# Kernel optimization log

Measured on AMD Instinct MI355X. Metric: run time of the kernel, lower is better.

The kernel has to match this reference:

```python
import jax, jax.numpy as jnp
import numpy as np

N_NODES = 50000
N_EDGES = 600000
F_IN = 128
HID = 128
N_CLASSES = 10
N_GRAPHS = 64


def _glorot(key, shape):
    fan_in, fan_out = shape[1], shape[0]
    lim = float(np.sqrt(6.0 / (fan_in + fan_out)))
    return jax.random.uniform(key, shape, jnp.float32, -lim, lim)


def setup_inputs() -> dict:
    key = jax.random.key(0)
    ks = jax.random.split(key, 16)
    x = jax.random.normal(ks[0], (N_NODES, F_IN), jnp.float32)
    edge_index = jax.random.randint(ks[1], (2, N_EDGES), 0, N_NODES, jnp.int64)
    batch = jnp.sort(jax.random.randint(ks[2], (N_NODES,), 0, N_GRAPHS, jnp.int64))
    # GraphConv params: lin_rel (with bias) applied to aggregated neighbor sum,
    # lin_root (no bias) applied to the node's own features.
    params = dict(
        W1_rel=_glorot(ks[3], (HID, F_IN)), b1_rel=jnp.zeros((HID,), jnp.float32),
        W1_root=_glorot(ks[4], (HID, F_IN)),
        W2_rel=_glorot(ks[5], (HID, HID)), b2_rel=jnp.zeros((HID,), jnp.float32),
        W2_root=_glorot(ks[6], (HID, HID)),
        W3_rel=_glorot(ks[7], (HID, HID)), b3_rel=jnp.zeros((HID,), jnp.float32),
        W3_root=_glorot(ks[8], (HID, HID)),
        W_lin=_glorot(ks[9], (N_CLASSES, HID)), b_lin=jnp.zeros((N_CLASSES,), jnp.float32),
    )
    return {"x": x, "edge_index": edge_index, "batch": batch, **params}


def _graph_conv(x, src, dst, W_rel, b_rel, W_root):
    # gather source features, scatter-add into targets, then linear (sum aggr
    # commutes with the linear, matching PyG GraphConv which applies lin_rel
    # after aggregation)
    agg = jax.ops.segment_sum(x[src], dst, num_segments=N_NODES)  # [N, F]
    return agg @ W_rel.T + b_rel + x @ W_root.T


def _mean_pool(x, batch):
    sums = jax.ops.segment_sum(x, batch, num_segments=N_GRAPHS)  # [G, H]
    cnts = jax.ops.segment_sum(jnp.ones((x.shape[0],), x.dtype), batch,
                               num_segments=N_GRAPHS)
    return sums / jnp.maximum(cnts, 1.0)[:, None]


def reference(x, edge_index, batch,
              W1_rel, b1_rel, W1_root,
              W2_rel, b2_rel, W2_root,
              W3_rel, b3_rel, W3_root,
              W_lin, b_lin):
    src, dst = edge_index[0], edge_index[1]
    h = jax.nn.relu(_graph_conv(x, src, dst, W1_rel, b1_rel, W1_root))
    h = jax.nn.relu(_graph_conv(h, src, dst, W2_rel, b2_rel, W2_root))
    h = _graph_conv(h, src, dst, W3_rel, b3_rel, W3_root)
    g = _mean_pool(h, batch)  # [G, H]
    # dropout is identity in eval mode (training=False)
    return g @ W_lin.T + b_lin  # [G, num_classes]
```

## Files before the change

kernel.cpp:

```cpp
#include <hip/hip_runtime.h>
#include <hip/hip_bf16.h>

#define N_NODES   50000
#define N_EDGES   600000
#define F         128
#define N_GRAPHS  64
#define N_CLASSES 10
#define NPAD      50048
#define NB_SCAN   196
#define XCVT_BLOCKS 6250
#define WCVT_BLOCKS 96
#define EDGE_BLOCKS 2344

typedef __attribute__((ext_vector_type(8))) short bf16x8;
typedef __attribute__((ext_vector_type(4))) float f32x4;

static __device__ __forceinline__ unsigned short f2bf(float f) {
    __hip_bfloat16 h = __float2bfloat16(f);
    return *reinterpret_cast<unsigned short*>(&h);
}
static __device__ __forceinline__ float bf2f(unsigned short u) {
    return __uint_as_float(((unsigned)u) << 16);
}

__global__ __launch_bounds__(256) void prep_kernel(
    const float* __restrict__ x,
    const float* __restrict__ W0, const float* __restrict__ W1,
    const float* __restrict__ W2, const float* __restrict__ W3,
    const float* __restrict__ W4, const float* __restrict__ W5,
    const int* __restrict__ dst,
    unsigned short* __restrict__ Xb, unsigned short* __restrict__ Wb,
    int* __restrict__ deg)
{
    int b = blockIdx.x;
    if (b < XCVT_BLOCKS) {
        int i = b * 256 + threadIdx.x;
        float4 v = reinterpret_cast<const float4*>(x)[i];
        ushort4 o;
        o.x = f2bf(v.x); o.y = f2bf(v.y); o.z = f2bf(v.z); o.w = f2bf(v.w);
        reinterpret_cast<ushort4*>(Xb)[i] = o;
    } else if (b < XCVT_BLOCKS + WCVT_BLOCKS) {
        const int PER = (F * F / 4) / 256;
        int bb  = b - XCVT_BLOCKS;
        int mat = bb / PER;
        int i   = (bb % PER) * 256 + threadIdx.x;
        const float* W = (mat == 0) ? W0 : (mat == 1) ? W1 : (mat == 2) ? W2
                       : (mat == 3) ? W3 : (mat == 4) ? W4 : W5;
        float4 v = reinterpret_cast<const float4*>(W)[i];
        ushort4 o;
        o.x = f2bf(v.x); o.y = f2bf(v.y); o.z = f2bf(v.z); o.w = f2bf(v.w);
        reinterpret_cast<ushort4*>(Wb + (size_t)mat * F * F)[i] = o;
    } else {
        int e = (b - XCVT_BLOCKS - WCVT_BLOCKS) * 256 + threadIdx.x;
        if (e < N_EDGES) atomicAdd(&deg[dst[e]], 1);
    }
}

__global__ __launch_bounds__(256) void scanA_kernel(
    const int* __restrict__ deg, int* __restrict__ locEx, int* __restrict__ blockSum)
{
    __shared__ int sh[256];
    int t = threadIdx.x;
    int idx = blockIdx.x * 256 + t;
    int v = (idx < N_NODES) ? deg[idx] : 0;
    sh[t] = v;
    __syncthreads();
#pragma unroll
    for (int d = 1; d < 256; d <<= 1) {
        int u = (t >= d) ? sh[t - d] : 0;
        __syncthreads();
        sh[t] += u;
        __syncthreads();
    }
    if (idx < N_NODES) locEx[idx] = sh[t] - v;
    if (t == 255) blockSum[blockIdx.x] = sh[255];
}

__global__ __launch_bounds__(256) void scanBC_kernel(
    const int* __restrict__ locEx, const int* __restrict__ blockSum,
    int* __restrict__ off)
{
    __shared__ int sh[256];
    int t = threadIdx.x;
    int v = (t < NB_SCAN) ? blockSum[t] : 0;
    sh[t] = v;
    __syncthreads();
#pragma unroll
    for (int d = 1; d < 256; d <<= 1) {
        int u = (t >= d) ? sh[t - d] : 0;
        __syncthreads();
        sh[t] += u;
        __syncthreads();
    }
    int myVal = blockSum[blockIdx.x];
    int base  = sh[blockIdx.x] - myVal;
    int idx = blockIdx.x * 256 + t;
    if (idx < N_NODES) off[idx] = locEx[idx] + base;
    if (blockIdx.x == 0 && t == 0) off[N_NODES] = sh[NB_SCAN - 1];
}

__global__ __launch_bounds__(256) void fillP_kernel(
    const int* __restrict__ src, const int* __restrict__ dst,
    const int* __restrict__ off, int* __restrict__ cursor,
    int* __restrict__ csrP)
{
    int e = blockIdx.x * 256 + threadIdx.x;
    if (e >= N_EDGES) return;
    int d = dst[e];
    int slot = atomicAdd(&cursor[d], 1);
    csrP[off[d] + slot] = src[e];
}

template <int RELU>
__global__ __launch_bounds__(256) void conv_fused(
    const unsigned short* __restrict__ Xb,
    const int* __restrict__ off, const int* __restrict__ csrP,
    const unsigned short* __restrict__ Wrel, const unsigned short* __restrict__ Wroot,
    const float* __restrict__ brel, unsigned short* __restrict__ H)
{
    __shared__ char AsRaw[64 * 256];
    const int t = threadIdx.x;
    const int mBase = blockIdx.x * 64;

    {
        const int r = t >> 2;
        const int q = t & 3;
        int row = mBase + r;
        float acc[32];
#pragma unroll
        for (int i = 0; i < 32; ++i) acc[i] = 0.f;
        if (row < N_NODES) {
            int j0 = off[row], j1 = off[row + 1];
            const int* lst = csrP;
            const unsigned short* Xq = Xb + (size_t)q * 32;
            int j = j0;
            for (; j + 2 <= j1; j += 2) {
                int sa = lst[j], sb = lst[j + 1];
                const bf16x8* pa = reinterpret_cast<const bf16x8*>(Xq + (size_t)sa * F);
                const bf16x8* pb = reinterpret_cast<const bf16x8*>(Xq + (size_t)sb * F);
                bf16x8 va0 = pa[0], va1 = pa[1], va2 = pa[2], va3 = pa[3];
                bf16x8 vb0 = pb[0], vb1 = pb[1], vb2 = pb[2], vb3 = pb[3];
#pragma unroll
                for (int e = 0; e < 8; ++e) {
                    acc[e]      += bf2f((unsigned short)va0[e]) + bf2f((unsigned short)vb0[e]);
                    acc[8 + e]  += bf2f((unsigned short)va1[e]) + bf2f((unsigned short)vb1[e]);
                    acc[16 + e] += bf2f((unsigned short)va2[e]) + bf2f((unsigned short)vb2[e]);
                    acc[24 + e] += bf2f((unsigned short)va3[e]) + bf2f((unsigned short)vb3[e]);
                }
            }
            if (j < j1) {
                int sa = lst[j];
                const bf16x8* pa = reinterpret_cast<const bf16x8*>(Xq + (size_t)sa * F);
                bf16x8 va0 = pa[0], va1 = pa[1], va2 = pa[2], va3 = pa[3];
#pragma unroll
                for (int e = 0; e < 8; ++e) {
                    acc[e]      += bf2f((unsigned short)va0[e]);
                    acc[8 + e]  += bf2f((unsigned short)va1[e]);
                    acc[16 + e] += bf2f((unsigned short)va2[e]);
                    acc[24 + e] += bf2f((unsigned short)va3[e]);
                }
            }
        }
#pragma unroll
        for (int cc = 0; cc < 4; ++cc) {
            bf16x8 o;
#pragma unroll
            for (int e = 0; e < 8; ++e) o[e] = (short)f2bf(acc[cc * 8 + e]);
            int bytecol = (q * 64 + cc * 16) ^ ((r & 7) << 4);
            *reinterpret_cast<bf16x8*>(AsRaw + r * 256 + bytecol) = o;
        }
    }
    __syncthreads();

    const int wave = t >> 6;
    const int lane = t & 63;
    const int wm = wave >> 1, wn = wave & 1;
    const int m0l = wm * 32;
    const int n0  = wn * 64;
    const int lrow = lane & 15;
    const int lk8  = (lane >> 4) << 3;

    f32x4 acc[2][4];
#pragma unroll
    for (int mi = 0; mi < 2; ++mi)
#pragma unroll
        for (int ni = 0; ni < 4; ++ni)
            acc[mi][ni] = (f32x4){0.f, 0.f, 0.f, 0.f};

#pragma unroll
    for (int p = 0; p < 2; ++p) {
        const unsigned short* W = p ? Wroot : Wrel;
#pragma unroll
        for (int ks = 0; ks < 4; ++ks) {
            int k0 = ks * 32 + lk8;
            bf16x8 a[2], b[4];
#pragma unroll
            for (int mi = 0; mi < 2; ++mi) {
                int rl = m0l + mi * 16 + lrow;
                if (p == 0) {
                    int bytecol = (k0 * 2) ^ ((rl & 7) << 4);
                    a[mi] = *reinterpret_cast<const bf16x8*>(AsRaw + rl * 256 + bytecol);
                } else {
                    a[mi] = *reinterpret_cast<const bf16x8*>(
                        Xb + (size_t)(mBase + rl) * F + k0);
                }
            }
#pragma unroll
            for (int ni = 0; ni < 4; ++ni)
                b[ni] = *reinterpret_cast<const bf16x8*>(
                    W + (size_t)(n0 + ni * 16 + lrow) * F + k0);
#pragma unroll
            for (int mi = 0; mi < 2; ++mi)
#pragma unroll
                for (int ni = 0; ni < 4; ++ni)
                    acc[mi][ni] = __builtin_amdgcn_mfma_f32_16x16x32_bf16(
                        a[mi], b[ni], acc[mi][ni], 0, 0, 0);
        }
    }

    const int r0 = (lane >> 4) << 2;
#pragma unroll
    for (int ni = 0; ni < 4; ++ni) {
        int col = n0 + ni * 16 + lrow;
        float bb = brel[col];
#pragma unroll
        for (int mi = 0; mi < 2; ++mi) {
#pragma unroll
            for (int r = 0; r < 4; ++r) {
                int row = mBase + m0l + mi * 16 + r0 + r;
                if (row < N_NODES) {
                    float v = acc[mi][ni][r] + bb;
                    if (RELU) v = fmaxf(v, 0.f);
                    H[(size_t)row * F + col] = f2bf(v);
                }
            }
        }
    }
}

__global__ __launch_bounds__(256) void poolhead_kernel(
    const unsigned short* __restrict__ H, const int* __restrict__ batch,
    const float* __restrict__ Wl, const float* __restrict__ bl,
    float* __restrict__ out)
{
    int g = blockIdx.x;
    int lo = 0, hi = N_NODES;
    while (lo < hi) { int m = (lo + hi) >> 1; if (batch[m] < g) lo = m + 1; else hi = m; }
    int start = lo;
    hi = N_NODES;
    while (lo < hi) { int m = (lo + hi) >> 1; if (batch[m] < g + 1) lo = m + 1; else hi = m; }
    int end = lo;

    int l8 = (threadIdx.x & 15) << 3;
    int rg = threadIdx.x >> 4;
    float acc[8] = {0.f, 0.f, 0.f, 0.f, 0.f, 0.f, 0.f, 0.f};
    for (int i = start + rg; i < end; i += 16) {
        bf16x8 v = *reinterpret_cast<const bf16x8*>(H + (size_t)i * F + l8);
#pragma unroll
        for (int r = 0; r < 8; ++r) acc[r] += bf2f((unsigned short)v[r]);
    }
    __shared__ float sh[16][F];
    __shared__ float mean[F];
#pragma unroll
    for (int r = 0; r < 8; ++r) sh[rg][l8 + r] = acc[r];
    __syncthreads();
    if (threadIdx.x < F) {
        int f = threadIdx.x;
        float s = 0.f;
#pragma unroll
        for (int k = 0; k < 16; ++k) s += sh[k][f];
        float cnt = (float)(end - start);
        mean[f] = s / fmaxf(cnt, 1.f);
    }
    __syncthreads();
    if (threadIdx.x < N_CLASSES) {
        int c = threadIdx.x;
        float s = bl[c];
#pragma unroll 8
        for (int k = 0; k < F; ++k) s += mean[k] * Wl[c * F + k];
        out[g * N_CLASSES + c] = s;
    }
}

extern "C" void kernel_launch(void* const* d_in, const int* in_sizes, int n_in,
                              void* d_out, int out_size, void* d_ws, size_t ws_size,
                              hipStream_t stream)
{
    const float* x     = (const float*)d_in[0];
    const int*   edge  = (const int*)d_in[1];
    const int*   src   = edge;
    const int*   dst   = edge + N_EDGES;
    const int*   batch = (const int*)d_in[2];
    const float* W1r = (const float*)d_in[3];
    const float* b1  = (const float*)d_in[4];
    const float* W1o = (const float*)d_in[5];
    const float* W2r = (const float*)d_in[6];
    const float* b2  = (const float*)d_in[7];
    const float* W2o = (const float*)d_in[8];
    const float* W3r = (const float*)d_in[9];
    const float* b3  = (const float*)d_in[10];
    const float* W3o = (const float*)d_in[11];
    const float* Wl  = (const float*)d_in[12];
    const float* bl  = (const float*)d_in[13];
    float* out = (float*)d_out;

    char* ws = (char*)d_ws;
    const size_t fb = (size_t)NPAD * F * sizeof(unsigned short);
    unsigned short* Xb  = (unsigned short*)ws;
    unsigned short* H1b = (unsigned short*)(ws + fb);
    unsigned short* H2b = (unsigned short*)(ws + 2 * fb);
    char* p = ws + 3 * fb;
    unsigned short* Wb = (unsigned short*)p;
    p += (size_t)6 * F * F * sizeof(unsigned short);
    int* deg     = (int*)p;              p += (size_t)N_NODES * sizeof(int);
    int* cursor  = (int*)p;              p += (size_t)N_NODES * sizeof(int);
    int* off     = (int*)p;              p += (size_t)(N_NODES + 1) * sizeof(int);
    int* locEx   = (int*)p;              p += (size_t)N_NODES * sizeof(int);
    int* blockSum= (int*)p;              p += (size_t)256 * sizeof(int);
    int* csrP    = (int*)p;              p += (size_t)N_EDGES * sizeof(int);

    const int convBlocks = NPAD / 64;
    const int prepBlocks = XCVT_BLOCKS + WCVT_BLOCKS + EDGE_BLOCKS;

    hipMemsetAsync(deg, 0, (size_t)2 * N_NODES * sizeof(int), stream);
    prep_kernel<<<prepBlocks, 256, 0, stream>>>(x, W1r, W1o, W2r, W2o, W3r, W3o,
                                                dst, Xb, Wb, deg);
    scanA_kernel<<<NB_SCAN, 256, 0, stream>>>(deg, locEx, blockSum);
    scanBC_kernel<<<NB_SCAN, 256, 0, stream>>>(locEx, blockSum, off);
    fillP_kernel<<<EDGE_BLOCKS, 256, 0, stream>>>(src, dst, off, cursor, csrP);

    conv_fused<1><<<convBlocks, 256, 0, stream>>>(Xb,  off, csrP, Wb + 0 * F * F, Wb + 1 * F * F, b1, H1b);
    conv_fused<1><<<convBlocks, 256, 0, stream>>>(H1b, off, csrP, Wb + 2 * F * F, Wb + 3 * F * F, b2, H2b);
    conv_fused<0><<<convBlocks, 256, 0, stream>>>(H2b, off, csrP, Wb + 4 * F * F, Wb + 5 * F * F, b3, H1b);

    poolhead_kernel<<<N_GRAPHS, 256, 0, stream>>>(H1b, batch, Wl, bl, out);
}
```

Baseline: 268.3 us.

## Store CSR neighbor indices as 16-bit and remap gather to 16 lanes per row

Neighbor indices in the CSR list are now stored as unsigned short instead of int. This halves index traffic and is valid because the node count fits in 16 bits. The aggregation phase of the fused conv kernel is reorganized: 16 threads now cover one 128-feature row, each loading 16 bytes per neighbor, and each thread walks 4 rows in sequence with a 4-way unrolled edge loop. This is meant to make the feature gathers more coalesced and to cut index bandwidth. In exchange, each thread has fewer independent loads in flight per row, and the 16-bit indices assume fewer than 65536 nodes.

```diff
diff --git a/kernel.cpp b/kernel.cpp
--- a/kernel.cpp
+++ b/kernel.cpp
@@ -102,19 +102,19 @@
 __global__ __launch_bounds__(256) void fillP_kernel(
     const int* __restrict__ src, const int* __restrict__ dst,
     const int* __restrict__ off, int* __restrict__ cursor,
-    int* __restrict__ csrP)
+    unsigned short* __restrict__ csrP)
 {
     int e = blockIdx.x * 256 + threadIdx.x;
     if (e >= N_EDGES) return;
     int d = dst[e];
     int slot = atomicAdd(&cursor[d], 1);
-    csrP[off[d] + slot] = src[e];
+    csrP[off[d] + slot] = (unsigned short)src[e];
 }
 
 template <int RELU>
 __global__ __launch_bounds__(256) void conv_fused(
     const unsigned short* __restrict__ Xb,
-    const int* __restrict__ off, const int* __restrict__ csrP,
+    const int* __restrict__ off, const unsigned short* __restrict__ csrP,
     const unsigned short* __restrict__ Wrel, const unsigned short* __restrict__ Wroot,
     const float* __restrict__ brel, unsigned short* __restrict__ H)
 {
@@ -123,50 +123,41 @@
     const int mBase = blockIdx.x * 64;
 
     {
-        const int r = t >> 2;
-        const int q = t & 3;
-        int row = mBase + r;
-        float acc[32];
-#pragma unroll
-        for (int i = 0; i < 32; ++i) acc[i] = 0.f;
-        if (row < N_NODES) {
-            int j0 = off[row], j1 = off[row + 1];
-            const int* lst = csrP;
-            const unsigned short* Xq = Xb + (size_t)q * 32;
-            int j = j0;
-            for (; j + 2 <= j1; j += 2) {
-                int sa = lst[j], sb = lst[j + 1];
-                const bf16x8* pa = reinterpret_cast<const bf16x8*>(Xq + (size_t)sa * F);
-                const bf16x8* pb = reinterpret_cast<const bf16x8*>(Xq + (size_t)sb * F);
-                bf16x8 va0 = pa[0], va1 = pa[1], va2 = pa[2], va3 = pa[3];
-                bf16x8 vb0 = pb[0], vb1 = pb[1], vb2 = pb[2], vb3 = pb[3];
-#pragma unroll
-                for (int e = 0; e < 8; ++e) {
-                    acc[e]      += bf2f((unsigned short)va0[e]) + bf2f((unsigned short)vb0[e]);
-                    acc[8 + e]  += bf2f((unsigned short)va1[e]) + bf2f((unsigned short)vb1[e]);
-                    acc[16 + e] += bf2f((unsigned short)va2[e]) + bf2f((unsigned short)vb2[e]);
-                    acc[24 + e] += bf2f((unsigned short)va3[e]) + bf2f((unsigned short)vb3[e]);
+        const int sub = t & 15;
+        const int rr  = t >> 4;
+        const unsigned short* Xq = Xb + sub * 8;
+#pragma unroll
+        for (int it = 0; it < 4; ++it) {
+            int r   = it * 16 + rr;
+            int row = mBase + r;
+            float acc[8] = {0.f, 0.f, 0.f, 0.f, 0.f, 0.f, 0.f, 0.f};
+            if (row < N_NODES) {
+                int j  = off[row];
+                int j1 = off[row + 1];
+                for (; j + 4 <= j1; j += 4) {
+                    int s0 = csrP[j], s1 = csrP[j + 1];
+                    int s2 = csrP[j + 2], s3 = csrP[j + 3];
+                    bf16x8 v0 = *reinterpret_cast<const bf16x8*>(Xq + (size_t)s0 * F);
+                    bf16x8 v1 = *reinterpret_cast<const bf16x8*>(Xq + (size_t)s1 * F);
+                    bf16x8 v2 = *reinterpret_cast<const bf16x8*>(Xq + (size_t)s2 * F);
+                    bf16x8 v3 = *reinterpret_cast<const bf16x8*>(Xq + (size_t)s3 * F);
+#pragma unroll
+                    for (int e = 0; e < 8; ++e) {
+                        acc[e] += (bf2f((unsigned short)v0[e]) + bf2f((unsigned short)v1[e]))
+                                + (bf2f((unsigned short)v2[e]) + bf2f((unsigned short)v3[e]));
+                    }
+                }
+                for (; j < j1; ++j) {
+                    int s0 = csrP[j];
+                    bf16x8 v0 = *reinterpret_cast<const bf16x8*>(Xq + (size_t)s0 * F);
+#pragma unroll
+                    for (int e = 0; e < 8; ++e) acc[e] += bf2f((unsigned short)v0[e]);
                 }
             }
-            if (j < j1) {
-                int sa = lst[j];
-                const bf16x8* pa = reinterpret_cast<const bf16x8*>(Xq + (size_t)sa * F);
-                bf16x8 va0 = pa[0], va1 = pa[1], va2 = pa[2], va3 = pa[3];
-#pragma unroll
-                for (int e = 0; e < 8; ++e) {
-                    acc[e]      += bf2f((unsigned short)va0[e]);
-                    acc[8 + e]  += bf2f((unsigned short)va1[e]);
-                    acc[16 + e] += bf2f((unsigned short)va2[e]);
-                    acc[24 + e] += bf2f((unsigned short)va3[e]);
-                }
-            }
-        }
-#pragma unroll
-        for (int cc = 0; cc < 4; ++cc) {
             bf16x8 o;
 #pragma unroll
-            for (int e = 0; e < 8; ++e) o[e] = (short)f2bf(acc[cc * 8 + e]);
-            int bytecol = (q * 64 + cc * 16) ^ ((r & 7) << 4);
+            for (int e = 0; e < 8; ++e) o[e] = (short)f2bf(acc[e]);
+            int bytecol = (sub * 16) ^ ((r & 7) << 4);
             *reinterpret_cast<bf16x8*>(AsRaw + r * 256 + bytecol) = o;
         }
     }
@@ -317,7 +308,7 @@
     int* off     = (int*)p;              p += (size_t)(N_NODES + 1) * sizeof(int);
     int* locEx   = (int*)p;              p += (size_t)N_NODES * sizeof(int);
     int* blockSum= (int*)p;              p += (size_t)256 * sizeof(int);
-    int* csrP    = (int*)p;              p += (size_t)N_EDGES * sizeof(int);
+    unsigned short* csrP = (unsigned short*)p;
 
     const int convBlocks = NPAD / 64;
     const int prepBlocks = XCVT_BLOCKS + WCVT_BLOCKS + EDGE_BLOCKS;
```

Result: faster. 241.3 us (-10.1%).
